# Optimization experiments

Hardware: AMD Instinct MI355X
Metric: run time of the kernel (lower is better)

Reference implementation:

```python
import jax, jax.numpy as jnp
import numpy as np

B, S, D = 2, 2048, 1024
H, DH, DM = 16, 64, 4096
EPS = 1e-5
IGNORE = -100000.0


def setup_inputs() -> dict:
    key = jax.random.key(0)
    ks = jax.random.split(key, 14)
    s = 0.02
    return {
        "x": jax.random.normal(ks[0], (B, S, D), jnp.float32),
        "W_Q": jax.random.normal(ks[1], (H, DH, D), jnp.float32) * s,
        "W_K": jax.random.normal(ks[2], (H, DH, D), jnp.float32) * s,
        "W_V": jax.random.normal(ks[3], (H, DH, D), jnp.float32) * s,
        "W_O": jax.random.normal(ks[4], (H, D, DH), jnp.float32) * s,
        "b_Q": jax.random.normal(ks[5], (H, DH), jnp.float32) * s,
        "b_K": jax.random.normal(ks[6], (H, DH), jnp.float32) * s,
        "b_V": jax.random.normal(ks[7], (H, DH), jnp.float32) * s,
        "b_O": jax.random.normal(ks[8], (D,), jnp.float32) * s,
        "W_in": jax.random.normal(ks[9], (DM, D), jnp.float32) * s,
        "b_in": jax.random.normal(ks[10], (DM,), jnp.float32) * s,
        "W_out": jax.random.normal(ks[11], (D, DM), jnp.float32) * s,
        "b_out": jax.random.normal(ks[12], (D,), jnp.float32) * s,
    }


def ln_pre(x):
    x = x - jnp.mean(x, axis=-1, keepdims=True)
    scale = jnp.sqrt(jnp.mean(x * x, axis=-1, keepdims=True) + EPS)
    return x / scale


def gelu_new(x):
    c = np.sqrt(2.0 / np.pi).astype(np.float32)
    return 0.5 * x * (1.0 + jnp.tanh(c * (x + 0.044715 * x ** 3)))


def reference(x, W_Q, W_K, W_V, W_O, b_Q, b_K, b_V, b_O, W_in, b_in, W_out, b_out):
    resid_pre = x
    xn = ln_pre(resid_pre)
    # q,k,v: [B, S, H, DH]
    q = jnp.einsum('ihm,bpm->bpih', W_Q, xn) + b_Q
    k = jnp.einsum('ihm,bpm->bpih', W_K, xn) + b_K
    v = jnp.einsum('ihm,bpm->bpih', W_V, xn) + b_V
    attn_scale = np.sqrt(DH).astype(np.float32)
    # scores: [B, H, Sq, Sk]  (einsum 'bpih,bqih->bipq')
    scores = jnp.einsum('bpih,bqih->bipq', q, k) / attn_scale
    mask = jnp.tril(jnp.ones((S, S), bool))
    scores = jnp.where(mask, scores, IGNORE)
    attn = jax.nn.softmax(scores, axis=-1)
    # z: [B, Sq, H, DH]
    z = jnp.einsum('bpih,biqp->bqih', v, attn)
    attn_out = jnp.einsum('idh,bqih->bqd', W_O, z) + b_O
    resid_mid = resid_pre + attn_out
    m = ln_pre(resid_mid)
    pre = jnp.einsum('md,bpd->bpm', W_in, m) + b_in
    post = gelu_new(pre)
    mlp_out = jnp.einsum('dm,bpm->bpd', W_out, post) + b_out
    return resid_mid + mlp_out
```

## Files before the change

kernel.cpp:

```cpp
#include <hip/hip_runtime.h>

typedef unsigned short u16;
typedef __attribute__((ext_vector_type(8))) short short8;
typedef __attribute__((ext_vector_type(4))) unsigned short ushort4v;
typedef __attribute__((ext_vector_type(4))) float float4v;

__device__ __forceinline__ float bf2f(u16 u) {
  union { unsigned int i; float f; } c; c.i = ((unsigned int)u) << 16; return c.f;
}
__device__ __forceinline__ u16 f2bf(float f) {
  union { float f; unsigned int i; } c; c.f = f;
  unsigned int u = c.i;
  return (u16)((u + 0x7fffu + ((u >> 16) & 1u)) >> 16);
}
__device__ __forceinline__ unsigned int cvt_pk_bf16(float a, float b) {
  unsigned int r;
  asm("v_cvt_pk_bf16_f32 %0, %1, %2" : "=v"(r) : "v"(a), "v"(b));
  return r;
}
__device__ __forceinline__ float gelu_new(float x) {
  const float k1 = 2.30218776f;
  const float k3 = 0.10294233f;
  float x3 = x * x * x;
  float e = __builtin_amdgcn_exp2f(-(k1 * x + k3 * x3));
  return x / (1.0f + e);
}
__device__ __forceinline__ float ldres(const float* p) { return *p; }
__device__ __forceinline__ float ldres(const u16* p) { return bf2f(*p); }

__device__ __forceinline__ void gload_lds16(const u16* g, u16* l) {
  __builtin_amdgcn_global_load_lds(
      (const __attribute__((address_space(1))) unsigned int*)g,
      (__attribute__((address_space(3))) unsigned int*)l, 16, 0, 0);
}

__global__ void cvt_bf16_multi(const float* __restrict__ s0, const float* __restrict__ s1,
                               const float* __restrict__ s2, const float* __restrict__ s3,
                               const float* __restrict__ s4, u16* __restrict__ d0,
                               u16* __restrict__ d1, u16* __restrict__ d2,
                               u16* __restrict__ d3, u16* __restrict__ d4) {
  int bid = blockIdx.x;
  const float* src; u16* dst; int base;
  if (bid < 512)       { src = s0; dst = d0; base = 0; }
  else if (bid < 1024) { src = s1; dst = d1; base = 512; }
  else if (bid < 1536) { src = s2; dst = d2; base = 1024; }
  else if (bid < 3584) { src = s3; dst = d3; base = 1536; }
  else                 { src = s4; dst = d4; base = 3584; }
  int t = (bid - base) * 256 + threadIdx.x;
  float4v a = *(const float4v*)(src + (size_t)t * 8);
  float4v b = *(const float4v*)(src + (size_t)t * 8 + 4);
  short8 o;
#pragma unroll
  for (int j = 0; j < 4; ++j) o[j] = (short)f2bf(a[j]);
#pragma unroll
  for (int j = 0; j < 4; ++j) o[4 + j] = (short)f2bf(b[j]);
  *(short8*)(dst + (size_t)t * 8) = o;
}

__global__ void prep_wo(const float* __restrict__ WO, u16* __restrict__ Wot) {
  int t = blockIdx.x * 256 + threadIdx.x;
  int i = t >> 13;
  int d = (t >> 3) & 1023;
  int h0 = (t & 7) * 8;
  const float* src = WO + (size_t)i * 65536 + d * 64 + h0;
  float4v a = *(const float4v*)(src);
  float4v b = *(const float4v*)(src + 4);
  short8 o;
#pragma unroll
  for (int j = 0; j < 4; ++j) o[j] = (short)f2bf(a[j]);
#pragma unroll
  for (int j = 0; j < 4; ++j) o[4 + j] = (short)f2bf(b[j]);
  *(short8*)(Wot + (size_t)d * 1024 + i * 64 + h0) = o;
}

__global__ void prep_bqkv(const float* __restrict__ bQ, const float* __restrict__ bK,
                          const float* __restrict__ bV, float* __restrict__ bqkv) {
  int t = blockIdx.x * 256 + threadIdx.x;
  if (t < 3072)
    bqkv[t] = (t < 1024) ? bQ[t] : (t < 2048) ? bK[t - 1024] : bV[t - 2048];
}

__global__ void ln_f32(const float* __restrict__ x, u16* __restrict__ y) {
  __shared__ float red1[4];
  __shared__ float red2[4];
  int token = blockIdx.x;
  int tid = threadIdx.x;
  int w = tid >> 6;
  const float* xr = x + (size_t)token * 1024;
  float4v v = *(const float4v*)(xr + tid * 4);
  float s = v[0] + v[1] + v[2] + v[3];
#pragma unroll
  for (int m = 32; m >= 1; m >>= 1) s += __shfl_xor(s, m);
  if ((tid & 63) == 0) red1[w] = s;
  __syncthreads();
  float mean = (red1[0] + red1[1] + red1[2] + red1[3]) * (1.0f / 1024.0f);
  float ss = 0.0f;
#pragma unroll
  for (int j = 0; j < 4; ++j) { v[j] -= mean; ss += v[j] * v[j]; }
#pragma unroll
  for (int m = 32; m >= 1; m >>= 1) ss += __shfl_xor(ss, m);
  if ((tid & 63) == 0) red2[w] = ss;
  __syncthreads();
  float ms = (red2[0] + red2[1] + red2[2] + red2[3]) * (1.0f / 1024.0f);
  float inv = 1.0f / sqrtf(ms + 1e-5f);
  ushort4v o;
#pragma unroll
  for (int j = 0; j < 4; ++j) o[j] = f2bf(v[j] * inv);
  *(ushort4v*)(y + (size_t)token * 1024 + tid * 4) = o;
}

template <int BN, int BK, bool GELU, bool VSPLIT, bool DBUF, typename TO, typename TR>
__global__ __launch_bounds__(256) void gemm_bt(
    const u16* __restrict__ A, const u16* __restrict__ Bw,
    const float* __restrict__ bias, const TR* __restrict__ resid,
    TO* __restrict__ C, u16* __restrict__ vTout, int M, int N, int K,
    int lda, int ldc) {
  constexpr int BM = 128;
  constexpr int SEGS = BK / 8;
  constexpr int SMASK = SEGS - 1;
  constexpr int FI = 4, FJ = BN / 32;
  constexpr int CA = BM * SEGS / 256;
  constexpr int CB = BN * SEGS / 256;
  constexpr int NB = DBUF ? 2 : 1;
  __shared__ __align__(16) u16 As[NB][BM * BK];
  __shared__ __align__(16) u16 Bs[NB][BN * BK];
  const int tid = threadIdx.x;
  const int w = tid >> 6, lane = tid & 63;
  const int quad = lane >> 4, l16 = lane & 15;
  const int m0 = blockIdx.x * BM, n0 = blockIdx.y * BN;
  const int wm = (w >> 1) * 64, wn = (w & 1) * (BN / 2);
  const int rmask = l16 & SMASK;
  float4v acc[FI][FJ] = {};

  auto stage = [&](int buf, int k0) {
#pragma unroll
    for (int t = 0; t < CA; ++t) {
      int chunk = (w * CA + t) * 64 + lane;
      int row = chunk / SEGS, seg = chunk % SEGS;
      int sseg = seg ^ (row & SMASK);
      gload_lds16(A + (size_t)(m0 + row) * lda + k0 + sseg * 8,
                  As[buf] + (w * CA + t) * 512);
    }
#pragma unroll
    for (int t = 0; t < CB; ++t) {
      int chunk = (w * CB + t) * 64 + lane;
      int row = chunk / SEGS, seg = chunk % SEGS;
      int sseg = seg ^ (row & SMASK);
      gload_lds16(Bw + (size_t)(n0 + row) * K + k0 + sseg * 8,
                  Bs[buf] + (w * CB + t) * 512);
    }
  };
  auto compute = [&](int buf) {
#pragma unroll
    for (int kk = 0; kk < BK; kk += 32) {
      short8 a[FI], b[FJ];
#pragma unroll
      for (int fi = 0; fi < FI; ++fi)
        a[fi] = *(const short8*)(As[buf] + (wm + fi * 16 + l16) * BK +
                                 ((((kk >> 3) + quad) ^ rmask) << 3));
#pragma unroll
      for (int fj = 0; fj < FJ; ++fj)
        b[fj] = *(const short8*)(Bs[buf] + (wn + fj * 16 + l16) * BK +
                                 ((((kk >> 3) + quad) ^ rmask) << 3));
#pragma unroll
      for (int fi = 0; fi < FI; ++fi)
#pragma unroll
        for (int fj = 0; fj < FJ; ++fj)
          acc[fi][fj] = __builtin_amdgcn_mfma_f32_16x16x32_bf16(
              a[fi], b[fj], acc[fi][fj], 0, 0, 0);
    }
  };

  if constexpr (DBUF) {
    stage(0, 0);
    __syncthreads();
    int cur = 0;
    for (int k0 = 0; k0 < K; k0 += BK) {
      if (k0 + BK < K) stage(cur ^ 1, k0 + BK);
      compute(cur);
      __syncthreads();
      cur ^= 1;
    }
  } else {
    for (int k0 = 0; k0 < K; k0 += BK) {
      __syncthreads();
      stage(0, k0);
      __syncthreads();
      compute(0);
    }
  }

#pragma unroll
  for (int fi = 0; fi < FI; ++fi) {
#pragma unroll
    for (int fj = 0; fj < FJ; ++fj) {
      int col = n0 + wn + fj * 16 + l16;
      float bv = bias ? bias[col] : 0.0f;
#pragma unroll
      for (int r = 0; r < 4; ++r) {
        int row = m0 + wm + fi * 16 + quad * 4 + r;
        float val = acc[fi][fj][r] + bv;
        if (resid) val += ldres(resid + (size_t)row * N + col);
        if (GELU) val = gelu_new(val);
        if (VSPLIT && col < 1024) val *= 0.18033688011112042f;
        if (VSPLIT && col >= 2048) {
          vTout[(size_t)(col - 2048) * 4096 + row] = f2bf(val);
        } else if constexpr (sizeof(TO) == 2) {
          C[(size_t)row * ldc + col] = f2bf(val);
        } else {
          C[(size_t)row * ldc + col] = val;
        }
      }
    }
  }
}

template <bool GELU>
__global__ __launch_bounds__(512, 2) void gemm256(
    const u16* __restrict__ A, const u16* __restrict__ Bw,
    const float* __restrict__ bias, u16* __restrict__ C,
    int M, int N, int K, int lda, int ldc) {
  constexpr int BK = 32;
  __shared__ __align__(16) u16 As[3][256 * BK];
  __shared__ __align__(16) u16 Bs[3][256 * BK];
  const int tid = threadIdx.x;
  const int w = tid >> 6, lane = tid & 63;
  const int quad = lane >> 4, l16 = lane & 15;
  const int rmask = l16 & 3;
  const int id = blockIdx.x;
  const int xcd = id & 7, local = id >> 3;
  const int mt = (xcd & 3) * 4 + (local >> 3);
  const int nt = (xcd >> 2) * 8 + (local & 7);
  const int m0 = mt * 256, n0 = nt * 256;
  const int wm = (w >> 2) * 128;
  const int wn = (w & 3) * 64;

  const u16* aSrc[2];
  const u16* bSrc[2];
#pragma unroll
  for (int i = 0; i < 2; ++i) {
    int chunk = (w * 2 + i) * 64 + lane;
    int row = chunk >> 2, pos = chunk & 3;
    int sseg = pos ^ (row & 3);
    aSrc[i] = A + (size_t)(m0 + row) * lda + sseg * 8;
    bSrc[i] = Bw + (size_t)(n0 + row) * K + sseg * 8;
  }

  float4v acc[8][4] = {};

  auto stage = [&](int buf, int t) {
#pragma unroll
    for (int i = 0; i < 2; ++i)
      gload_lds16(aSrc[i] + t * BK, &As[buf][(w * 2 + i) * 512]);
#pragma unroll
    for (int i = 0; i < 2; ++i)
      gload_lds16(bSrc[i] + t * BK, &Bs[buf][(w * 2 + i) * 512]);
  };
  auto compute = [&](int buf) {
    short8 a_[8], b_[4];
#pragma unroll
    for (int mi = 0; mi < 8; ++mi)
      a_[mi] = *(const short8*)(&As[buf][(wm + mi * 16 + l16) * BK +
                                         ((quad ^ rmask) << 3)]);
#pragma unroll
    for (int ni = 0; ni < 4; ++ni)
      b_[ni] = *(const short8*)(&Bs[buf][(wn + ni * 16 + l16) * BK +
                                         ((quad ^ rmask) << 3)]);
    __builtin_amdgcn_s_setprio(1);
#pragma unroll
    for (int mi = 0; mi < 8; ++mi)
#pragma unroll
      for (int ni = 0; ni < 4; ++ni)
        acc[mi][ni] = __builtin_amdgcn_mfma_f32_16x16x32_bf16(
            a_[mi], b_[ni], acc[mi][ni], 0, 0, 0);
    __builtin_amdgcn_s_setprio(0);
  };

  const int ntk = K >> 5;
  stage(0, 0);
  stage(1, 1);
  stage(2, 2);
  asm volatile("s_waitcnt vmcnt(8)" ::: "memory");
  asm volatile("s_barrier" ::: "memory");

  int buf = 0;
  for (int t = 0; t < ntk; ++t) {
    compute(buf);
    if (t == ntk - 1) break;
    asm volatile("s_waitcnt lgkmcnt(0)" ::: "memory");
    asm volatile("s_barrier" ::: "memory");
    if (t + 3 < ntk) {
      stage(buf, t + 3);
      asm volatile("s_waitcnt vmcnt(8)" ::: "memory");
    } else if (t + 2 < ntk) {
      asm volatile("s_waitcnt vmcnt(4)" ::: "memory");
    } else {
      asm volatile("s_waitcnt vmcnt(0)" ::: "memory");
    }
    asm volatile("s_barrier" ::: "memory");
    buf = (buf == 2) ? 0 : buf + 1;
  }

#pragma unroll
  for (int mi = 0; mi < 8; ++mi) {
#pragma unroll
    for (int ni = 0; ni < 4; ++ni) {
      int col = n0 + wn + ni * 16 + l16;
      float bv = bias[col];
#pragma unroll
      for (int r = 0; r < 4; ++r) {
        int row = m0 + wm + mi * 16 + quad * 4 + r;
        float val = acc[mi][ni][r] + bv;
        if (GELU) val = gelu_new(val);
        C[(size_t)row * ldc + col] = f2bf(val);
      }
    }
  }
}

__global__ __launch_bounds__(256) void attn_flash(u16* __restrict__ qk,
                                                  const u16* __restrict__ vT) {
  constexpr int PADK = 72;
  constexpr float THR2 = 10.0f;
  __shared__ __align__(16) u16 Ks[64 * PADK];
  __shared__ __align__(16) u16 Vt[64 * PADK];
  __shared__ __align__(16) u16 Ps[4][16 * PADK];
  const int id = blockIdx.x;
  const int qt = 31 - (id >> 5);
  const int combo = id & 31;
  const int head = combo >> 1, b = combo & 1;
  const int tid = threadIdx.x;
  const int w = tid >> 6, lane = tid & 63;
  const int quad = lane >> 4, l16 = lane & 15;
  const int q0 = qt * 64;
  const size_t tokB = (size_t)b * 2048;

  short8 aq[2];
#pragma unroll
  for (int ks = 0; ks < 2; ++ks)
    aq[ks] = *(const short8*)(qk + (tokB + q0 + w * 16 + l16) * 2048 +
                              head * 64 + ks * 32 + quad * 8);

  const u16* kbase = qk + tokB * 2048 + 1024 + head * 64;
  const u16* vbase = vT + (size_t)head * 64 * 4096 + tokB;

  short8 bones = {};
  if (l16 == 0) {
#pragma unroll
    for (int j = 0; j < 8; ++j) bones[j] = (short)0x3F80;
  }

  float m_st[4] = {-1e30f, -1e30f, -1e30f, -1e30f};
  float4v o_acc[4] = {};
  float4v o5 = {0.f, 0.f, 0.f, 0.f};

  const int srow = tid >> 2;
  const int sseg = (tid & 3) * 2;
  const u16* kptr = kbase + (size_t)srow * 2048 + sseg * 8;
  const u16* vptr = vbase + (size_t)srow * 4096 + sseg * 8;
  u16* ksl = Ks + srow * PADK + sseg * 8;
  u16* vsl = Vt + srow * PADK + sseg * 8;

  short8 pk0 = *(const short8*)(kptr);
  short8 pk1 = *(const short8*)(kptr + 8);
  short8 pv0 = *(const short8*)(vptr);
  short8 pv1 = *(const short8*)(vptr + 8);

  for (int kt = 0; kt <= qt; ++kt) {
    const int kk0 = kt * 64;
    __syncthreads();
    *(short8*)(ksl) = pk0;
    *(short8*)(ksl + 8) = pk1;
    *(short8*)(vsl) = pv0;
    *(short8*)(vsl + 8) = pv1;
    __syncthreads();
    if (kt < qt) {
      const u16* kp = kptr + (size_t)(kk0 + 64) * 2048;
      const u16* vp = vptr + kk0 + 64;
      pk0 = *(const short8*)(kp);
      pk1 = *(const short8*)(kp + 8);
      pv0 = *(const short8*)(vp);
      pv1 = *(const short8*)(vp + 8);
    }

    float4v s[4];
    __builtin_amdgcn_s_setprio(1);
#pragma unroll
    for (int fj = 0; fj < 4; ++fj) {
      float4v t = {0.f, 0.f, 0.f, 0.f};
#pragma unroll
      for (int ks = 0; ks < 2; ++ks) {
        short8 bk = *(const short8*)(Ks + (fj * 16 + l16) * PADK + ks * 32 + quad * 8);
        t = __builtin_amdgcn_mfma_f32_16x16x32_bf16(aq[ks], bk, t, 0, 0, 0);
      }
      s[fj] = t;
    }
    __builtin_amdgcn_s_setprio(0);
    if (kt == qt) {
#pragma unroll
      for (int fj = 0; fj < 4; ++fj) {
        int col = kk0 + fj * 16 + l16;
#pragma unroll
        for (int r = 0; r < 4; ++r) {
          int row = q0 + w * 16 + quad * 4 + r;
          if (col > row) s[fj][r] = -1e30f;
        }
      }
    }
    float mx[4];
#pragma unroll
    for (int r = 0; r < 4; ++r) {
      float m = fmaxf(fmaxf(s[0][r], s[1][r]), fmaxf(s[2][r], s[3][r]));
      m = fmaxf(m, __shfl_xor(m, 1));
      m = fmaxf(m, __shfl_xor(m, 2));
      m = fmaxf(m, __shfl_xor(m, 4));
      m = fmaxf(m, __shfl_xor(m, 8));
      mx[r] = m;
    }
    bool need = false;
#pragma unroll
    for (int r = 0; r < 4; ++r) need |= (mx[r] > m_st[r] + THR2);
    if (__any(need)) {
#pragma unroll
      for (int r = 0; r < 4; ++r) {
        float mnew = fmaxf(m_st[r], mx[r]);
        float al = __builtin_amdgcn_exp2f(m_st[r] - mnew);
        m_st[r] = mnew;
        o5[r] *= al;
#pragma unroll
        for (int fj = 0; fj < 4; ++fj) o_acc[fj][r] *= al;
      }
    }
#pragma unroll
    for (int fj = 0; fj < 4; ++fj) {
#pragma unroll
      for (int r = 0; r < 4; r += 2) {
        float e0 = __builtin_amdgcn_exp2f(s[fj][r] - m_st[r]);
        float e1 = __builtin_amdgcn_exp2f(s[fj][r + 1] - m_st[r + 1]);
        unsigned int pp = cvt_pk_bf16(e0, e1);
        Ps[w][(quad * 4 + r) * PADK + fj * 16 + l16] = (u16)pp;
        Ps[w][(quad * 4 + r + 1) * PADK + fj * 16 + l16] = (u16)(pp >> 16);
      }
    }
    short8 ap[2];
#pragma unroll
    for (int ks = 0; ks < 2; ++ks)
      ap[ks] = *(const short8*)(&Ps[w][l16 * PADK + ks * 32 + quad * 8]);
    __builtin_amdgcn_s_setprio(1);
#pragma unroll
    for (int fj = 0; fj < 4; ++fj)
#pragma unroll
      for (int ks = 0; ks < 2; ++ks) {
        short8 bv = *(const short8*)(Vt + (fj * 16 + l16) * PADK + ks * 32 + quad * 8);
        o_acc[fj] = __builtin_amdgcn_mfma_f32_16x16x32_bf16(ap[ks], bv, o_acc[fj], 0, 0, 0);
      }
#pragma unroll
    for (int ks = 0; ks < 2; ++ks)
      o5 = __builtin_amdgcn_mfma_f32_16x16x32_bf16(ap[ks], bones, o5, 0, 0, 0);
    __builtin_amdgcn_s_setprio(0);
  }
#pragma unroll
  for (int r = 0; r < 4; ++r) {
    float lsum = __shfl(o5[r], lane & 48);
    float inv = 1.0f / lsum;
    int row = q0 + w * 16 + quad * 4 + r;
#pragma unroll
    for (int fj = 0; fj < 4; ++fj)
      qk[(tokB + row) * 2048 + head * 64 + fj * 16 + l16] =
          f2bf(o_acc[fj][r] * inv);
  }
}

extern "C" void kernel_launch(void* const* d_in, const int* in_sizes, int n_in,
                              void* d_out, int out_size, void* d_ws, size_t ws_size,
                              hipStream_t stream) {
  const float* x = (const float*)d_in[0];
  const float* W_Q = (const float*)d_in[1];
  const float* W_K = (const float*)d_in[2];
  const float* W_V = (const float*)d_in[3];
  const float* W_O = (const float*)d_in[4];
  const float* b_Q = (const float*)d_in[5];
  const float* b_K = (const float*)d_in[6];
  const float* b_V = (const float*)d_in[7];
  const float* b_O = (const float*)d_in[8];
  const float* W_in = (const float*)d_in[9];
  const float* b_in = (const float*)d_in[10];
  const float* W_out = (const float*)d_in[11];
  const float* b_out = (const float*)d_in[12];
  float* out = (float*)d_out;

  char* ws = (char*)d_ws;
  u16* Wqkv = (u16*)(ws);
  u16* Wot  = (u16*)(ws + 6291456);
  u16* Wib  = (u16*)(ws + 8388608);
  u16* Wob  = (u16*)(ws + 16777216);
  float* bqkv = (float*)(ws + 25165824);
  u16* xn   = (u16*)(ws + 25178112);
  u16* qk   = (u16*)(ws + 33566720);
  u16* vT   = (u16*)(ws + 50343936);
  u16* hbuf = (u16*)(ws + 33566720);
  float* rm = (float*)(ws + 67121152);

  cvt_bf16_multi<<<5632, 256, 0, stream>>>(W_Q, W_K, W_V, W_in, W_out,
                                           Wqkv, Wqkv + 1048576, Wqkv + 2097152,
                                           Wib, Wob);
  prep_wo<<<512, 256, 0, stream>>>(W_O, Wot);
  prep_bqkv<<<12, 256, 0, stream>>>(b_Q, b_K, b_V, bqkv);

  ln_f32<<<4096, 256, 0, stream>>>(x, xn);
  gemm_bt<128, 64, false, true, false, u16, float><<<dim3(32, 24), 256, 0, stream>>>(
      xn, Wqkv, bqkv, (const float*)nullptr, qk, vT, 4096, 3072, 1024, 1024, 2048);
  attn_flash<<<1024, 256, 0, stream>>>(qk, vT);
  gemm_bt<64, 64, false, false, true, float, float><<<dim3(32, 16), 256, 0, stream>>>(
      qk , Wot, b_O, x, rm, nullptr, 4096, 1024, 1024, 2048, 1024);
  ln_f32<<<4096, 256, 0, stream>>>(rm, xn);
  gemm256<true><<<256, 512, 0, stream>>>(xn, Wib, b_in, hbuf,
                                         4096, 4096, 1024, 1024, 4096);
  gemm_bt<64, 64, false, false, true, float, float><<<dim3(32, 16), 256, 0, stream>>>(
      hbuf, Wob, b_out, rm, out, nullptr, 4096, 1024, 4096, 4096, 1024);
}
```

Before: 358.5 us.

## Use 1024-thread 256x256 GEMM with split-K for MLP down projection

```diff
diff --git a/kernel.cpp b/kernel.cpp
--- a/kernel.cpp
+++ b/kernel.cpp
@@ -107,6 +107,24 @@
 #pragma unroll
   for (int j = 0; j < 4; ++j) o[j] = f2bf(v[j] * inv);
   *(ushort4v*)(y + (size_t)token * 1024 + tid * 4) = o;
+}
+
+__global__ void reduce_mlp(float* __restrict__ out, const u16* __restrict__ p1,
+                           const u16* __restrict__ p2, const u16* __restrict__ p3) {
+  size_t t = (size_t)blockIdx.x * 256 + threadIdx.x;
+  float4v o0 = *(float4v*)(out + t * 8);
+  float4v o1 = *(float4v*)(out + t * 8 + 4);
+  short8 a = *(const short8*)(p1 + t * 8);
+  short8 b = *(const short8*)(p2 + t * 8);
+  short8 c = *(const short8*)(p3 + t * 8);
+#pragma unroll
+  for (int j = 0; j < 4; ++j)
+    o0[j] += bf2f((u16)a[j]) + bf2f((u16)b[j]) + bf2f((u16)c[j]);
+#pragma unroll
+  for (int j = 0; j < 4; ++j)
+    o1[j] += bf2f((u16)a[4 + j]) + bf2f((u16)b[4 + j]) + bf2f((u16)c[4 + j]);
+  *(float4v*)(out + t * 8) = o0;
+  *(float4v*)(out + t * 8 + 4) = o1;
 }
 
 template <int BN, int BK, bool GELU, bool VSPLIT, bool DBUF, typename TO, typename TR>
@@ -215,11 +233,13 @@
   }
 }
 
-template <bool GELU>
-__global__ __launch_bounds__(512, 2) void gemm256(
+template <bool GELU, bool SPLITK>
+__global__ __launch_bounds__(1024, 4) void gemm256k(
     const u16* __restrict__ A, const u16* __restrict__ Bw,
-    const float* __restrict__ bias, u16* __restrict__ C,
-    int M, int N, int K, int lda, int ldc) {
+    const float* __restrict__ bias, const float* __restrict__ resid,
+    float* __restrict__ outF, u16* __restrict__ outB,
+    u16* __restrict__ p1, u16* __restrict__ p2, u16* __restrict__ p3,
+    int lda, int ldb, int ldc) {
   constexpr int BK = 32;
   __shared__ __align__(16) u16 As[3][256 * BK];
   __shared__ __align__(16) u16 Bs[3][256 * BK];
@@ -227,39 +247,34 @@
   const int w = tid >> 6, lane = tid & 63;
   const int quad = lane >> 4, l16 = lane & 15;
   const int rmask = l16 & 3;
-  const int id = blockIdx.x;
-  const int xcd = id & 7, local = id >> 3;
-  const int mt = (xcd & 3) * 4 + (local >> 3);
-  const int nt = (xcd >> 2) * 8 + (local & 7);
+  int mt, nt;
+  if constexpr (SPLITK) {
+    mt = blockIdx.x >> 2; nt = blockIdx.x & 3;
+  } else {
+    const int id = blockIdx.x;
+    const int xcd = id & 7, local = id >> 3;
+    mt = (xcd & 3) * 4 + (local >> 3);
+    nt = (xcd >> 2) * 8 + (local & 7);
+  }
   const int m0 = mt * 256, n0 = nt * 256;
-  const int wm = (w >> 2) * 128;
-  const int wn = (w & 3) * 64;
-
-  const u16* aSrc[2];
-  const u16* bSrc[2];
-#pragma unroll
-  for (int i = 0; i < 2; ++i) {
-    int chunk = (w * 2 + i) * 64 + lane;
-    int row = chunk >> 2, pos = chunk & 3;
-    int sseg = pos ^ (row & 3);
-    aSrc[i] = A + (size_t)(m0 + row) * lda + sseg * 8;
-    bSrc[i] = Bw + (size_t)(n0 + row) * K + sseg * 8;
-  }
-
-  float4v acc[8][4] = {};
+  const int wm = (w >> 2) * 64, wn = (w & 3) * 64;
+  const int kBase = SPLITK ? blockIdx.y * 1024 : 0;
+
+  const int srow = tid >> 2, spos = tid & 3;
+  const int sseg = spos ^ (srow & 3);
+  const u16* aSrc = A + (size_t)(m0 + srow) * lda + kBase + sseg * 8;
+  const u16* bSrc = Bw + (size_t)(n0 + srow) * ldb + kBase + sseg * 8;
+
+  float4v acc[4][4] = {};
 
   auto stage = [&](int buf, int t) {
-#pragma unroll
-    for (int i = 0; i < 2; ++i)
-      gload_lds16(aSrc[i] + t * BK, &As[buf][(w * 2 + i) * 512]);
-#pragma unroll
-    for (int i = 0; i < 2; ++i)
-      gload_lds16(bSrc[i] + t * BK, &Bs[buf][(w * 2 + i) * 512]);
+    gload_lds16(aSrc + t * BK, &As[buf][tid * 8]);
+    gload_lds16(bSrc + t * BK, &Bs[buf][tid * 8]);
   };
   auto compute = [&](int buf) {
-    short8 a_[8], b_[4];
-#pragma unroll
-    for (int mi = 0; mi < 8; ++mi)
+    short8 a_[4], b_[4];
+#pragma unroll
+    for (int mi = 0; mi < 4; ++mi)
       a_[mi] = *(const short8*)(&As[buf][(wm + mi * 16 + l16) * BK +
                                          ((quad ^ rmask) << 3)]);
 #pragma unroll
@@ -268,7 +283,7 @@
                                          ((quad ^ rmask) << 3)]);
     __builtin_amdgcn_s_setprio(1);
 #pragma unroll
-    for (int mi = 0; mi < 8; ++mi)
+    for (int mi = 0; mi < 4; ++mi)
 #pragma unroll
       for (int ni = 0; ni < 4; ++ni)
         acc[mi][ni] = __builtin_amdgcn_mfma_f32_16x16x32_bf16(
@@ -276,11 +291,11 @@
     __builtin_amdgcn_s_setprio(0);
   };
 
-  const int ntk = K >> 5;
+  constexpr int ntk = 32;
   stage(0, 0);
   stage(1, 1);
   stage(2, 2);
-  asm volatile("s_waitcnt vmcnt(8)" ::: "memory");
+  asm volatile("s_waitcnt vmcnt(4)" ::: "memory");
   asm volatile("s_barrier" ::: "memory");
 
   int buf = 0;
@@ -291,9 +306,9 @@
     asm volatile("s_barrier" ::: "memory");
     if (t + 3 < ntk) {
       stage(buf, t + 3);
-      asm volatile("s_waitcnt vmcnt(8)" ::: "memory");
+      asm volatile("s_waitcnt vmcnt(4)" ::: "memory");
     } else if (t + 2 < ntk) {
-      asm volatile("s_waitcnt vmcnt(4)" ::: "memory");
+      asm volatile("s_waitcnt vmcnt(2)" ::: "memory");
     } else {
       asm volatile("s_waitcnt vmcnt(0)" ::: "memory");
     }
@@ -302,17 +317,27 @@
   }
 
 #pragma unroll
-  for (int mi = 0; mi < 8; ++mi) {
+  for (int mi = 0; mi < 4; ++mi) {
 #pragma unroll
     for (int ni = 0; ni < 4; ++ni) {
       int col = n0 + wn + ni * 16 + l16;
-      float bv = bias[col];
 #pragma unroll
       for (int r = 0; r < 4; ++r) {
         int row = m0 + wm + mi * 16 + quad * 4 + r;
-        float val = acc[mi][ni][r] + bv;
-        if (GELU) val = gelu_new(val);
-        C[(size_t)row * ldc + col] = f2bf(val);
+        float val = acc[mi][ni][r];
+        if constexpr (SPLITK) {
+          if (blockIdx.y == 0) {
+            outF[(size_t)row * ldc + col] =
+                val + bias[col] + resid[(size_t)row * ldc + col];
+          } else {
+            u16* pz = (blockIdx.y == 1) ? p1 : (blockIdx.y == 2) ? p2 : p3;
+            pz[(size_t)row * ldc + col] = f2bf(val);
+          }
+        } else {
+          val += bias[col];
+          if (GELU) val = gelu_new(val);
+          outB[(size_t)row * ldc + col] = f2bf(val);
+        }
       }
     }
   }
@@ -500,6 +525,9 @@
   u16* vT   = (u16*)(ws + 50343936);
   u16* hbuf = (u16*)(ws + 33566720);
   float* rm = (float*)(ws + 67121152);
+  u16* P1 = (u16*)(ws);
+  u16* P2 = (u16*)(ws + 8388608);
+  u16* P3 = (u16*)(ws + 25178112);
 
   cvt_bf16_multi<<<5632, 256, 0, stream>>>(W_Q, W_K, W_V, W_in, W_out,
                                            Wqkv, Wqkv + 1048576, Wqkv + 2097152,
@@ -514,8 +542,11 @@
   gemm_bt<64, 64, false, false, true, float, float><<<dim3(32, 16), 256, 0, stream>>>(
       qk , Wot, b_O, x, rm, nullptr, 4096, 1024, 1024, 2048, 1024);
   ln_f32<<<4096, 256, 0, stream>>>(rm, xn);
-  gemm256<true><<<256, 512, 0, stream>>>(xn, Wib, b_in, hbuf,
-                                         4096, 4096, 1024, 1024, 4096);
-  gemm_bt<64, 64, false, false, true, float, float><<<dim3(32, 16), 256, 0, stream>>>(
-      hbuf, Wob, b_out, rm, out, nullptr, 4096, 1024, 4096, 4096, 1024);
-}
+  gemm256k<true, false><<<dim3(256, 1), 1024, 0, stream>>>(
+      xn, Wib, b_in, nullptr, nullptr, hbuf, nullptr, nullptr, nullptr,
+      1024, 1024, 4096);
+  gemm256k<false, true><<<dim3(64, 4), 1024, 0, stream>>>(
+      hbuf, Wob, b_out, rm, out, nullptr, P1, P2, P3,
+      4096, 4096, 1024);
+  reduce_mlp<<<2048, 256, 0, stream>>>(out, P1, P2, P3);
+}
```

New measurement: 365.6 us. No clear change (+2.0%).
